# Optimization experiments

Measured on AMD Instinct MI355X. Metric: run time of the kernel, lower is better.

The kernel has to match this reference:

```python
import jax, jax.numpy as jnp
import numpy as np

MGC_SIZE = 80
COND_DIM = 256
LSTM_SIZE = 500
UP_SCALE = 64  # prod([4,4,4])
TEMPERATURE = 1.0
EPS_MIN = -7.0


def setup_inputs() -> dict:
    key = jax.random.key(0)
    ks = jax.random.split(key, 10)
    B, T_FRAMES = 16, 32
    T = T_FRAMES * UP_SCALE  # 2048 decode steps
    s = 0.02  # weight scale for numerical stability (logvar goes through exp)
    return {
        "mgc": jax.random.normal(ks[0], (B, T_FRAMES, MGC_SIZE), dtype=jnp.float32),
        "eps": jax.random.normal(ks[1], (B, T), dtype=jnp.float32),
        # UpsampleNet stand-in: linear projection mgc_size->256, then repeat x64 in time
        "W_up": jax.random.normal(ks[2], (MGC_SIZE, COND_DIM), dtype=jnp.float32) * s,
        "b_up": jnp.zeros((COND_DIM,), dtype=jnp.float32),
        # LSTM (PyTorch layout, gate order i,f,g,o)
        "W_ih": jax.random.normal(ks[3], (4 * LSTM_SIZE, COND_DIM + 1), dtype=jnp.float32) * s,
        "W_hh": jax.random.normal(ks[4], (4 * LSTM_SIZE, LSTM_SIZE), dtype=jnp.float32) * s,
        "b_ih": jax.random.normal(ks[5], (4 * LSTM_SIZE,), dtype=jnp.float32) * s,
        "b_hh": jax.random.normal(ks[6], (4 * LSTM_SIZE,), dtype=jnp.float32) * s,
        # output Linear(lstm_size, 2)
        "W_out": jax.random.normal(ks[7], (2, LSTM_SIZE), dtype=jnp.float32) * s,
        "b_out": jnp.zeros((2,), dtype=jnp.float32),
    }


def reference(mgc, eps, W_up, b_up, W_ih, W_hh, b_ih, b_hh, W_out, b_out):
    B = mgc.shape[0]
    # conditioning: (B, T_frames, 80) -> (B, T, 256)
    cond = jnp.repeat(mgc @ W_up + b_up, UP_SCALE, axis=1)
    bias = b_ih + b_hh

    def step(carry, xs):
        h, c, x_prev = carry              # (B,H), (B,H), (B,)
        cond_t, eps_t = xs                # (B,256), (B,)
        inp = jnp.concatenate([cond_t, x_prev[:, None]], axis=1)  # (B,257)
        gates = inp @ W_ih.T + h @ W_hh.T + bias                  # (B,4H)
        i, f, g, o = jnp.split(gates, 4, axis=1)
        i = jax.nn.sigmoid(i)
        f = jax.nn.sigmoid(f)
        g = jnp.tanh(g)
        o = jax.nn.sigmoid(o)
        c = f * c + i * g
        h = o * jnp.tanh(c)
        out = h @ W_out.T + b_out         # (B,2)
        mean = jnp.tanh(out[:, 0])
        logvar = jnp.maximum(out[:, 1], EPS_MIN)  # clamp(min=eps_min)
        zz = mean + (eps_t * TEMPERATURE) * jnp.exp(logvar)
        return (h, c, zz), (mean, logvar, zz)

    h0 = jnp.zeros((B, LSTM_SIZE), dtype=mgc.dtype)
    c0 = jnp.zeros((B, LSTM_SIZE), dtype=mgc.dtype)
    x0 = jnp.zeros((B,), dtype=mgc.dtype)
    xs = (cond.transpose(1, 0, 2), eps.T)  # time-major
    _, (mean, logvar, zz) = jax.lax.scan(step, (h0, c0, x0), xs)
    # back to (B, T)
    return mean.T, logvar.T, zz.T
```

## Files before the change

kernel.cpp:

```cpp
#include <hip/hip_runtime.h>
#include <stdint.h>

#define TSTEPS 2048
#define NB     16
#define HDIM   500
#define NSLICE 16
#define NTHR   256
#define RECU32 320
#define REC64  160
#define GSTR   20

typedef __attribute__((ext_vector_type(8))) short s16x8;
typedef __attribute__((ext_vector_type(4))) float f32x4;

__device__ __forceinline__ unsigned short f2bf(float f) {
    unsigned u = __float_as_uint(f);
    u += 0x7FFFu + ((u >> 16) & 1u);
    return (unsigned short)(u >> 16);
}
__device__ __forceinline__ float sigm(float x)   { return __fdividef(1.f, 1.f + __expf(-x)); }
__device__ __forceinline__ float tanhf_(float x) { return 1.f - __fdividef(2.f, __expf(2.f * x) + 1.f); }

__global__ void zero_ws_kernel(uint32_t* p, int n) {
    int i = blockIdx.x * blockDim.x + threadIdx.x;
    if (i < n) p[i] = 0u;
}

__global__ __launch_bounds__(NTHR, 1) void wavernn_persist(
    const float* __restrict__ mgc,  const float* __restrict__ eps,
    const float* __restrict__ Wup,  const float* __restrict__ bup,
    const float* __restrict__ Wih,  const float* __restrict__ Whh,
    const float* __restrict__ bih,  const float* __restrict__ bhh,
    const float* __restrict__ Wout, const float* __restrict__ bout,
    float* __restrict__ out, uint32_t* __restrict__ hbuf, uint32_t* __restrict__ seq)
{
    const int s    = blockIdx.x;
    const int tid  = threadIdx.x;
    const int lane = tid & 63;
    const int wave = tid >> 6;
    const int l16  = lane & 15;
    const int g    = lane >> 4;

    __shared__ __align__(16) float gates_l[NB * 132];
    __shared__ __align__(16) float gcond[128 * GSTR];
    __shared__ __align__(16) float condT[256 * NB];
    __shared__ __align__(16) float mgcl[NB * 80];
    __shared__ __align__(16) float eps_l[128 * NB];
    __shared__ __align__(16) float zz_l[NB];

    uint64_t* hb64all = (uint64_t*)hbuf;

    s16x8 bfr[2][16];
    float wihl[2];
    #pragma unroll
    for (int t2 = 0; t2 < 2; ++t2) {
        const int q    = t2 * 16 + l16;
        const int hidx = s * 32 + q;
        const bool valid = hidx < HDIM;
        const int grow = wave * HDIM + hidx;
        wihl[t2] = valid ? Wih[grow * 257 + 256] : 0.f;
        #pragma unroll
        for (int kk = 0; kk < 16; ++kk) {
            const int k0 = kk * 32 + g * 8;
            s16x8 r;
            #pragma unroll
            for (int j = 0; j < 8; ++j) {
                const int k = k0 + j;
                const float v = (valid && k < HDIM) ? Whh[grow * HDIM + k] : 0.f;
                r[j] = (short)f2bf(v);
            }
            bfr[t2][kk] = r;
        }
    }
    const int b_e = tid >> 4;
    const int qh  = tid & 15;
    const int q0  = 2 * qh, q1 = q0 + 1;
    const int k0g = s * 32 + q0, k1g = s * 32 + q1;
    const float w0q0 = (k0g < HDIM) ? Wout[k0g]        : 0.f;
    const float w0q1 = (k1g < HDIM) ? Wout[k1g]        : 0.f;
    const float w1q0 = (k0g < HDIM) ? Wout[HDIM + k0g] : 0.f;
    const float w1q1 = (k1g < HDIM) ? Wout[HDIM + k1g] : 0.f;
    const float bout0 = bout[0], bout1 = bout[1];
    float cst0 = 0.f, cst1 = 0.f;

    auto rebuild = [&](int f) {
        for (int i = tid; i < NB * 80; i += NTHR) {
            const int b = i / 80, m = i - b * 80;
            mgcl[i] = mgc[(b * 32 + f) * 80 + m];
        }
        for (int i = tid; i < 64 * NB; i += NTHR) {
            const int st = i >> 4, b = i & 15;
            eps_l[((f & 1) * 64 + st) * NB + b] = eps[b * 2048 + f * 64 + st];
        }
        __syncthreads();
        {
            const int c = tid;
            float a[NB];
            #pragma unroll
            for (int b = 0; b < NB; ++b) a[b] = bup[c];
            for (int m = 0; m < 80; ++m) {
                const float w = Wup[m * 256 + c];
                #pragma unroll
                for (int b = 0; b < NB; ++b) a[b] += mgcl[b * 80 + m] * w;
            }
            #pragma unroll
            for (int b = 0; b < NB; ++b) condT[c * NB + b] = a[b];
        }
        __syncthreads();
        {
            const int n = tid >> 1, kc = tid & 1;
            const int gate = n >> 5, q = n & 31;
            const int hidx = s * 32 + q;
            const bool valid = hidx < HDIM;
            const int grow = gate * HDIM + hidx;
            float a[NB];
            #pragma unroll
            for (int b = 0; b < NB; ++b) a[b] = 0.f;
            if (valid) {
                const float* wr = Wih + (size_t)grow * 257 + kc * 128;
                for (int k = 0; k < 128; ++k) {
                    const float w = wr[k];
                    const float* cp = &condT[(kc * 128 + k) * NB];
                    #pragma unroll
                    for (int b = 0; b < NB; ++b) a[b] += cp[b] * w;
                }
            }
            if (kc == 0) {
                const float bias = valid ? (bih[grow] + bhh[grow]) : 0.f;
                #pragma unroll
                for (int b = 0; b < NB; ++b) gcond[n * GSTR + b] = a[b] + bias;
            }
            __syncthreads();
            if (kc == 1) {
                #pragma unroll
                for (int b = 0; b < NB; ++b) gcond[n * GSTR + b] += a[b];
            }
        }
        __syncthreads();
    };

    rebuild(0);

    for (int t = 0; t < TSTEPS; ++t) {
        if (t > 0) {
            if (lane < 16) {
                int guard = 0;
                while (__hip_atomic_load(&seq[lane * 32], __ATOMIC_RELAXED,
                                         __HIP_MEMORY_SCOPE_AGENT) < (uint32_t)t) {
                    if (++guard > (1 << 20)) break;
                }
            }
            asm volatile("" ::: "memory");
        }

        uint64_t* hb64 = hb64all + (size_t)(((t & 1) ^ 1) * 16) * REC64;
        s16x8 hfr[16];
        #pragma unroll
        for (int kk = 0; kk < 16; ++kk) {
            union { uint64_t u[2]; s16x8 v; } hu;
            hu.u[0] = __hip_atomic_load(hb64 + kk * REC64 + l16 * 8 + g * 2,
                                        __ATOMIC_RELAXED, __HIP_MEMORY_SCOPE_AGENT);
            hu.u[1] = __hip_atomic_load(hb64 + kk * REC64 + l16 * 8 + g * 2 + 1,
                                        __ATOMIC_RELAXED, __HIP_MEMORY_SCOPE_AGENT);
            hfr[kk] = hu.v;
        }
        uint64_t pv[4];
        if (t > 0) {
            #pragma unroll
            for (int j = 0; j < 4; ++j)
                pv[j] = __hip_atomic_load(hb64 + l16 * REC64 + 128 + g + 4 * j,
                                          __ATOMIC_RELAXED, __HIP_MEMORY_SCOPE_AGENT);
        }

        const int n0 = wave * 32 + l16;
        f32x4 acc0a = *(const f32x4*)&gcond[n0 * GSTR + g * 4];
        f32x4 acc1a = *(const f32x4*)&gcond[(n0 + 16) * GSTR + g * 4];
        f32x4 acc0b = {0.f, 0.f, 0.f, 0.f};
        f32x4 acc1b = {0.f, 0.f, 0.f, 0.f};
        #pragma unroll
        for (int kk = 0; kk < 8; ++kk) {
            acc0a = __builtin_amdgcn_mfma_f32_16x16x32_bf16(hfr[kk],     bfr[0][kk],     acc0a, 0, 0, 0);
            acc1a = __builtin_amdgcn_mfma_f32_16x16x32_bf16(hfr[kk],     bfr[1][kk],     acc1a, 0, 0, 0);
            acc0b = __builtin_amdgcn_mfma_f32_16x16x32_bf16(hfr[kk + 8], bfr[0][kk + 8], acc0b, 0, 0, 0);
            acc1b = __builtin_amdgcn_mfma_f32_16x16x32_bf16(hfr[kk + 8], bfr[1][kk + 8], acc1b, 0, 0, 0);
        }

        if (t > 0) {
            float o0[4], o1[4];
            #pragma unroll
            for (int j = 0; j < 4; ++j) {
                o0[j] = __uint_as_float((uint32_t)pv[j]);
                o1[j] = __uint_as_float((uint32_t)(pv[j] >> 32));
            }
            #pragma unroll
            for (int m = 1; m < 16; m <<= 1) {
                #pragma unroll
                for (int j = 0; j < 4; ++j) {
                    o0[j] += __shfl_xor(o0[j], m);
                    o1[j] += __shfl_xor(o1[j], m);
                }
            }
            const int row = (t - 1) & 127;
            float meanj[4], lvj[4], zzj[4];
            #pragma unroll
            for (int j = 0; j < 4; ++j) {
                const int B = g + 4 * j;
                meanj[j] = tanhf_(o0[j] + bout0);
                lvj[j]   = fmaxf(o1[j] + bout1, -7.f);
                zzj[j]   = meanj[j] + eps_l[row * NB + B] * __expf(lvj[j]);
            }
            if (l16 == 0) {
                #pragma unroll
                for (int j = 0; j < 4; ++j) zz_l[g + 4 * j] = zzj[j];
            }
            if (s == 0 && wave == 0 && l16 == 0) {
                #pragma unroll
                for (int j = 0; j < 4; ++j) {
                    const int B = g + 4 * j;
                    out[         B * 2048 + (t - 1)] = meanj[j];
                    out[32768 +  B * 2048 + (t - 1)] = lvj[j];
                    out[65536 +  B * 2048 + (t - 1)] = zzj[j];
                }
            }
        }

        f32x4 r0 = acc0a + acc0b;
        f32x4 r1 = acc1a + acc1b;
        if (t > 0) {
            const f32x4 zzq = *(const f32x4*)&zz_l[g * 4];
            r0 += zzq * wihl[0];
            r1 += zzq * wihl[1];
        }
        #pragma unroll
        for (int v = 0; v < 4; ++v) {
            gates_l[(g * 4 + v) * 132 + n0]      = r0[v];
            gates_l[(g * 4 + v) * 132 + n0 + 16] = r1[v];
        }
        __syncthreads();

        {
            float po0, po1;
            uint32_t hp = 0;
            {
                const float gi = gates_l[b_e * 132 +      q0];
                const float gf = gates_l[b_e * 132 + 32 + q0];
                const float gg = gates_l[b_e * 132 + 64 + q0];
                const float go = gates_l[b_e * 132 + 96 + q0];
                cst0 = sigm(gf) * cst0 + sigm(gi) * tanhf_(gg);
                const float h = sigm(go) * tanhf_(cst0);
                if (k0g < HDIM) hp |= (uint32_t)f2bf(h);
                po0 = h * w0q0; po1 = h * w1q0;
            }
            {
                const float gi = gates_l[b_e * 132 +      q1];
                const float gf = gates_l[b_e * 132 + 32 + q1];
                const float gg = gates_l[b_e * 132 + 64 + q1];
                const float go = gates_l[b_e * 132 + 96 + q1];
                cst1 = sigm(gf) * cst1 + sigm(gi) * tanhf_(gg);
                const float h = sigm(go) * tanhf_(cst1);
                if (k1g < HDIM) hp |= ((uint32_t)f2bf(h)) << 16;
                po0 += h * w0q1; po1 += h * w1q1;
            }
            const uint32_t rbase = (uint32_t)(((t & 1) * 16 + s) * RECU32);
            __hip_atomic_store(&hbuf[rbase + b_e * 16 + qh], hp,
                               __ATOMIC_RELAXED, __HIP_MEMORY_SCOPE_AGENT);
            po0 += __shfl_xor(po0, 1);  po1 += __shfl_xor(po1, 1);
            po0 += __shfl_xor(po0, 2);  po1 += __shfl_xor(po1, 2);
            po0 += __shfl_xor(po0, 4);  po1 += __shfl_xor(po1, 4);
            po0 += __shfl_xor(po0, 8);  po1 += __shfl_xor(po1, 8);
            if (qh == 0) {
                const uint64_t pk = (uint64_t)__float_as_uint(po0) |
                                    ((uint64_t)__float_as_uint(po1) << 32);
                __hip_atomic_store((uint64_t*)&hbuf[rbase + 256 + b_e * 2], pk,
                                   __ATOMIC_RELAXED, __HIP_MEMORY_SCOPE_AGENT);
            }
        }
        __syncthreads();
        if (tid == 0)
            __hip_atomic_store(&seq[s * 32], (uint32_t)(t + 1),
                               __ATOMIC_RELEASE, __HIP_MEMORY_SCOPE_AGENT);

        if (((t + 1) & 63) == 0 && (t + 1) < TSTEPS) rebuild((t + 1) >> 6);
    }

    if (s == 0 && wave == 0) {
        if (lane < 16) {
            int guard = 0;
            while (__hip_atomic_load(&seq[lane * 32], __ATOMIC_RELAXED,
                                     __HIP_MEMORY_SCOPE_AGENT) < (uint32_t)TSTEPS) {
                if (++guard > (1 << 20)) break;
            }
        }
        asm volatile("" ::: "memory");
        uint64_t* hb64 = hb64all + (size_t)16 * REC64;
        float o0[4], o1[4];
        #pragma unroll
        for (int j = 0; j < 4; ++j) {
            const uint64_t pvv = __hip_atomic_load(hb64 + l16 * REC64 + 128 + g + 4 * j,
                                                   __ATOMIC_RELAXED, __HIP_MEMORY_SCOPE_AGENT);
            o0[j] = __uint_as_float((uint32_t)pvv);
            o1[j] = __uint_as_float((uint32_t)(pvv >> 32));
        }
        #pragma unroll
        for (int m = 1; m < 16; m <<= 1) {
            #pragma unroll
            for (int j = 0; j < 4; ++j) {
                o0[j] += __shfl_xor(o0[j], m);
                o1[j] += __shfl_xor(o1[j], m);
            }
        }
        if (l16 == 0) {
            #pragma unroll
            for (int j = 0; j < 4; ++j) {
                const int B = g + 4 * j;
                const float mean = tanhf_(o0[j] + bout0);
                const float lvv  = fmaxf(o1[j] + bout1, -7.f);
                const float zzv  = mean + eps_l[127 * NB + B] * __expf(lvv);
                out[         B * 2048 + 2047] = mean;
                out[32768 +  B * 2048 + 2047] = lvv;
                out[65536 +  B * 2048 + 2047] = zzv;
            }
        }
    }
}

extern "C" void kernel_launch(void* const* d_in, const int* in_sizes, int n_in,
                              void* d_out, int out_size, void* d_ws, size_t ws_size,
                              hipStream_t stream) {
    const float* mgc  = (const float*)d_in[0];
    const float* eps  = (const float*)d_in[1];
    const float* Wup  = (const float*)d_in[2];
    const float* bup  = (const float*)d_in[3];
    const float* Wih  = (const float*)d_in[4];
    const float* Whh  = (const float*)d_in[5];
    const float* bih  = (const float*)d_in[6];
    const float* bhh  = (const float*)d_in[7];
    const float* Wout = (const float*)d_in[8];
    const float* bout = (const float*)d_in[9];

    uint32_t* hbuf = (uint32_t*)d_ws;
    uint32_t* seq  = hbuf + 32 * RECU32;

    zero_ws_kernel<<<42, 256, 0, stream>>>(hbuf, 32 * RECU32 + 512);
    wavernn_persist<<<NSLICE, NTHR, 0, stream>>>(mgc, eps, Wup, bup, Wih, Whh,
                                                 bih, bhh, Wout, bout,
                                                 (float*)d_out, hbuf, seq);
}
```

Before: 10.87 ms.

## Replace sequence-counter barrier with step-tagged 64-bit data words and LDS staging

Drops the per-block sequence counter, the release store and the trailing block barrier. Each published h word and output partial now carries the step number in its upper 32 bits, so consumers spin directly on the data until every tag matches, which removes the separate flag round trip from the critical path. The h tile is staged through swizzled LDS before the MFMA fragments are read, and the output-projection partials are packed as bf16. Costs are doubled global traffic per h word, lower precision for the mean/logvar partial sums, and reliance on 64-bit atomic store atomicity for correctness.

Measured after the change: 10.76 ms. Within noise of the previous version (-1.0%).

```diff
diff --git a/kernel.cpp b/kernel.cpp
--- a/kernel.cpp
+++ b/kernel.cpp
@@ -6,9 +6,10 @@
 #define HDIM   500
 #define NSLICE 16
 #define NTHR   256
-#define RECU32 320
-#define REC64  160
 #define GSTR   20
+
+#define HBASE(P) ((size_t)(P) * 4096)
+#define PBASE(P) (8192 + (size_t)(P) * 256)
 
 typedef __attribute__((ext_vector_type(8))) short s16x8;
 typedef __attribute__((ext_vector_type(4))) float f32x4;
@@ -18,6 +19,7 @@
     u += 0x7FFFu + ((u >> 16) & 1u);
     return (unsigned short)(u >> 16);
 }
+__device__ __forceinline__ float bf2f(uint32_t hw) { return __uint_as_float(hw << 16); }
 __device__ __forceinline__ float sigm(float x)   { return __fdividef(1.f, 1.f + __expf(-x)); }
 __device__ __forceinline__ float tanhf_(float x) { return 1.f - __fdividef(2.f, __expf(2.f * x) + 1.f); }
 
@@ -32,7 +34,7 @@
     const float* __restrict__ Wih,  const float* __restrict__ Whh,
     const float* __restrict__ bih,  const float* __restrict__ bhh,
     const float* __restrict__ Wout, const float* __restrict__ bout,
-    float* __restrict__ out, uint32_t* __restrict__ hbuf, uint32_t* __restrict__ seq)
+    float* __restrict__ out, uint64_t* __restrict__ hb)
 {
     const int s    = blockIdx.x;
     const int tid  = threadIdx.x;
@@ -41,14 +43,13 @@
     const int l16  = lane & 15;
     const int g    = lane >> 4;
 
+    __shared__ __align__(16) uint32_t h_l[16 * 16 * 16];
     __shared__ __align__(16) float gates_l[NB * 132];
     __shared__ __align__(16) float gcond[128 * GSTR];
     __shared__ __align__(16) float condT[256 * NB];
     __shared__ __align__(16) float mgcl[NB * 80];
     __shared__ __align__(16) float eps_l[128 * NB];
     __shared__ __align__(16) float zz_l[NB];
-
-    uint64_t* hb64all = (uint64_t*)hbuf;
 
     s16x8 bfr[2][16];
     float wihl[2];
@@ -139,36 +140,46 @@
         __syncthreads();
     };
 
+    for (int i = tid; i < 16 * 16 * 16; i += NTHR) h_l[i] = 0u;
     rebuild(0);
 
     for (int t = 0; t < TSTEPS; ++t) {
         if (t > 0) {
-            if (lane < 16) {
-                int guard = 0;
-                while (__hip_atomic_load(&seq[lane * 32], __ATOMIC_RELAXED,
-                                         __HIP_MEMORY_SCOPE_AGENT) < (uint32_t)t) {
-                    if (++guard > (1 << 20)) break;
-                }
-            }
-            asm volatile("" ::: "memory");
-        }
-
-        uint64_t* hb64 = hb64all + (size_t)(((t & 1) ^ 1) * 16) * REC64;
-        s16x8 hfr[16];
-        #pragma unroll
-        for (int kk = 0; kk < 16; ++kk) {
-            union { uint64_t u[2]; s16x8 v; } hu;
-            hu.u[0] = __hip_atomic_load(hb64 + kk * REC64 + l16 * 8 + g * 2,
-                                        __ATOMIC_RELAXED, __HIP_MEMORY_SCOPE_AGENT);
-            hu.u[1] = __hip_atomic_load(hb64 + kk * REC64 + l16 * 8 + g * 2 + 1,
-                                        __ATOMIC_RELAXED, __HIP_MEMORY_SCOPE_AGENT);
-            hfr[kk] = hu.v;
-        }
+            const int p = tid & 15, b = tid >> 4;
+            const uint64_t* src = hb + HBASE((t & 1) ^ 1) + (size_t)p * 256 + b * 16;
+            const uint32_t want = (uint32_t)t;
+            uint64_t v[16];
+            #pragma unroll
+            for (int i = 0; i < 16; ++i)
+                v[i] = __hip_atomic_load(src + i, __ATOMIC_RELAXED, __HIP_MEMORY_SCOPE_AGENT);
+            int guard = 0;
+            while (true) {
+                bool ok = true;
+                #pragma unroll
+                for (int i = 0; i < 16; ++i) ok &= ((uint32_t)(v[i] >> 32) == want);
+                if (ok || ++guard > (1 << 18)) break;
+                #pragma unroll
+                for (int i = 0; i < 16; ++i)
+                    v[i] = __hip_atomic_load(src + i, __ATOMIC_RELAXED, __HIP_MEMORY_SCOPE_AGENT);
+            }
+            const int sw = ((b ^ (b >> 2)) & 3) ^ (p & 3);
+            uint32_t* dst = &h_l[p * 256 + b * 16];
+            #pragma unroll
+            for (int q = 0; q < 4; ++q) {
+                uint4 w;
+                w.x = (uint32_t)v[4 * q + 0]; w.y = (uint32_t)v[4 * q + 1];
+                w.z = (uint32_t)v[4 * q + 2]; w.w = (uint32_t)v[4 * q + 3];
+                *(uint4*)&dst[(q ^ sw) * 4] = w;
+            }
+        }
+        __syncthreads();
+
         uint64_t pv[4];
         if (t > 0) {
+            const uint64_t* pb = hb + PBASE((t & 1) ^ 1);
             #pragma unroll
             for (int j = 0; j < 4; ++j)
-                pv[j] = __hip_atomic_load(hb64 + l16 * REC64 + 128 + g + 4 * j,
+                pv[j] = __hip_atomic_load(pb + l16 * 16 + (g + 4 * j),
                                           __ATOMIC_RELAXED, __HIP_MEMORY_SCOPE_AGENT);
         }
 
@@ -177,6 +188,12 @@
         f32x4 acc1a = *(const f32x4*)&gcond[(n0 + 16) * GSTR + g * 4];
         f32x4 acc0b = {0.f, 0.f, 0.f, 0.f};
         f32x4 acc1b = {0.f, 0.f, 0.f, 0.f};
+        s16x8 hfr[16];
+        #pragma unroll
+        for (int p = 0; p < 16; ++p) {
+            const int sw = ((l16 ^ (l16 >> 2)) & 3) ^ (p & 3);
+            hfr[p] = *(const s16x8*)&h_l[p * 256 + l16 * 16 + (g ^ sw) * 4];
+        }
         #pragma unroll
         for (int kk = 0; kk < 8; ++kk) {
             acc0a = __builtin_amdgcn_mfma_f32_16x16x32_bf16(hfr[kk],     bfr[0][kk],     acc0a, 0, 0, 0);
@@ -186,11 +203,24 @@
         }
 
         if (t > 0) {
+            const uint64_t* pb = hb + PBASE((t & 1) ^ 1);
+            const uint32_t want = (uint32_t)t;
+            int guard = 0;
+            while (true) {
+                bool ok = true;
+                #pragma unroll
+                for (int j = 0; j < 4; ++j) ok &= ((uint32_t)(pv[j] >> 32) == want);
+                if (ok || ++guard > (1 << 18)) break;
+                #pragma unroll
+                for (int j = 0; j < 4; ++j)
+                    pv[j] = __hip_atomic_load(pb + l16 * 16 + (g + 4 * j),
+                                              __ATOMIC_RELAXED, __HIP_MEMORY_SCOPE_AGENT);
+            }
             float o0[4], o1[4];
             #pragma unroll
             for (int j = 0; j < 4; ++j) {
-                o0[j] = __uint_as_float((uint32_t)pv[j]);
-                o1[j] = __uint_as_float((uint32_t)(pv[j] >> 32));
+                o0[j] = bf2f((uint32_t)pv[j] & 0xFFFFu);
+                o1[j] = bf2f(((uint32_t)pv[j]) >> 16);
             }
             #pragma unroll
             for (int m = 1; m < 16; m <<= 1) {
@@ -213,6 +243,7 @@
                 #pragma unroll
                 for (int j = 0; j < 4; ++j) zz_l[g + 4 * j] = zzj[j];
             }
+            __builtin_amdgcn_sched_barrier(0);
             if (s == 0 && wave == 0 && l16 == 0) {
                 #pragma unroll
                 for (int j = 0; j < 4; ++j) {
@@ -239,6 +270,7 @@
         __syncthreads();
 
         {
+            const uint64_t tag = ((uint64_t)(uint32_t)(t + 1)) << 32;
             float po0, po1;
             uint32_t hp = 0;
             {
@@ -261,45 +293,48 @@
                 if (k1g < HDIM) hp |= ((uint32_t)f2bf(h)) << 16;
                 po0 += h * w0q1; po1 += h * w1q1;
             }
-            const uint32_t rbase = (uint32_t)(((t & 1) * 16 + s) * RECU32);
-            __hip_atomic_store(&hbuf[rbase + b_e * 16 + qh], hp,
+            __hip_atomic_store(hb + HBASE(t & 1) + (size_t)s * 256 + b_e * 16 + qh,
+                               (uint64_t)hp | tag,
                                __ATOMIC_RELAXED, __HIP_MEMORY_SCOPE_AGENT);
             po0 += __shfl_xor(po0, 1);  po1 += __shfl_xor(po1, 1);
             po0 += __shfl_xor(po0, 2);  po1 += __shfl_xor(po1, 2);
             po0 += __shfl_xor(po0, 4);  po1 += __shfl_xor(po1, 4);
             po0 += __shfl_xor(po0, 8);  po1 += __shfl_xor(po1, 8);
             if (qh == 0) {
-                const uint64_t pk = (uint64_t)__float_as_uint(po0) |
-                                    ((uint64_t)__float_as_uint(po1) << 32);
-                __hip_atomic_store((uint64_t*)&hbuf[rbase + 256 + b_e * 2], pk,
+                const uint32_t pk = (uint32_t)f2bf(po0) | ((uint32_t)f2bf(po1) << 16);
+                __hip_atomic_store(hb + PBASE(t & 1) + s * 16 + b_e,
+                                   (uint64_t)pk | tag,
                                    __ATOMIC_RELAXED, __HIP_MEMORY_SCOPE_AGENT);
             }
         }
-        __syncthreads();
-        if (tid == 0)
-            __hip_atomic_store(&seq[s * 32], (uint32_t)(t + 1),
-                               __ATOMIC_RELEASE, __HIP_MEMORY_SCOPE_AGENT);
 
         if (((t + 1) & 63) == 0 && (t + 1) < TSTEPS) rebuild((t + 1) >> 6);
     }
 
     if (s == 0 && wave == 0) {
-        if (lane < 16) {
-            int guard = 0;
-            while (__hip_atomic_load(&seq[lane * 32], __ATOMIC_RELAXED,
-                                     __HIP_MEMORY_SCOPE_AGENT) < (uint32_t)TSTEPS) {
-                if (++guard > (1 << 20)) break;
-            }
-        }
-        asm volatile("" ::: "memory");
-        uint64_t* hb64 = hb64all + (size_t)16 * REC64;
+        const uint64_t* pb = hb + PBASE(1);
+        const uint32_t want = (uint32_t)TSTEPS;
+        uint64_t pv[4];
+        #pragma unroll
+        for (int j = 0; j < 4; ++j)
+            pv[j] = __hip_atomic_load(pb + l16 * 16 + (g + 4 * j),
+                                      __ATOMIC_RELAXED, __HIP_MEMORY_SCOPE_AGENT);
+        int guard = 0;
+        while (true) {
+            bool ok = true;
+            #pragma unroll
+            for (int j = 0; j < 4; ++j) ok &= ((uint32_t)(pv[j] >> 32) == want);
+            if (ok || ++guard > (1 << 18)) break;
+            #pragma unroll
+            for (int j = 0; j < 4; ++j)
+                pv[j] = __hip_atomic_load(pb + l16 * 16 + (g + 4 * j),
+                                          __ATOMIC_RELAXED, __HIP_MEMORY_SCOPE_AGENT);
+        }
         float o0[4], o1[4];
         #pragma unroll
         for (int j = 0; j < 4; ++j) {
-            const uint64_t pvv = __hip_atomic_load(hb64 + l16 * REC64 + 128 + g + 4 * j,
-                                                   __ATOMIC_RELAXED, __HIP_MEMORY_SCOPE_AGENT);
-            o0[j] = __uint_as_float((uint32_t)pvv);
-            o1[j] = __uint_as_float((uint32_t)(pvv >> 32));
+            o0[j] = bf2f((uint32_t)pv[j] & 0xFFFFu);
+            o1[j] = bf2f(((uint32_t)pv[j]) >> 16);
         }
         #pragma unroll
         for (int m = 1; m < 16; m <<= 1) {
@@ -338,11 +373,10 @@
     const float* Wout = (const float*)d_in[8];
     const float* bout = (const float*)d_in[9];
 
-    uint32_t* hbuf = (uint32_t*)d_ws;
-    uint32_t* seq  = hbuf + 32 * RECU32;
-
-    zero_ws_kernel<<<42, 256, 0, stream>>>(hbuf, 32 * RECU32 + 512);
+    uint64_t* hb = (uint64_t*)d_ws;
+
+    zero_ws_kernel<<<68, 256, 0, stream>>>((uint32_t*)hb, 17408);
     wavernn_persist<<<NSLICE, NTHR, 0, stream>>>(mgc, eps, Wup, bup, Wih, Whh,
                                                  bih, bhh, Wout, bout,
-                                                 (float*)d_out, hbuf, seq);
+                                                 (float*)d_out, hb);
 }
```
